# Performance work log

Measured on AMD Instinct MI355X. Metric: run time of the kernel, lower is better.

## Reference

```python
import jax, jax.numpy as jnp
import numpy as np


def _pe_2d(H, W, C, dtype):
    # PositionalEncodingPermute2D: returns (C, H, W)
    ch_half = (C + 1) // 2
    inv = 1.0 / (10000.0 ** (jnp.arange(0, ch_half, 2, dtype=jnp.float32) / ch_half))
    tH = jnp.arange(H, dtype=jnp.float32)
    tW = jnp.arange(W, dtype=jnp.float32)
    sinH = tH[:, None] * inv[None, :]              # (H, ch_half//2)
    sinW = tW[:, None] * inv[None, :]              # (W, ch_half//2)
    embH = jnp.concatenate([jnp.sin(sinH), jnp.cos(sinH)], axis=-1)  # (H, ch_half)
    embW = jnp.concatenate([jnp.sin(sinW), jnp.cos(sinW)], axis=-1)  # (W, ch_half)
    E = jnp.concatenate([
        jnp.broadcast_to(embW[None, :, :], (H, W, ch_half)),
        jnp.broadcast_to(embH[:, None, :], (H, W, ch_half)),
    ], axis=-1)[..., :C]                            # (H, W, C)
    return jnp.transpose(E, (2, 0, 1)).astype(dtype)  # (C, H, W)


def setup_inputs() -> dict:
    key = jax.random.key(0)
    k0, k1, k2, k3 = jax.random.split(key, 4)
    B, C, H, W = 4, 256, 64, 64
    s = 1.0 / np.sqrt(C)  # kaiming-ish scale
    return {
        "x": jax.random.normal(k0, (B, C, H, W), dtype=jnp.float32),
        "wq": jax.random.normal(k1, (C, C), dtype=jnp.float32) * s,
        "wk": jax.random.normal(k2, (C, C), dtype=jnp.float32) * s,
        "wv": jax.random.normal(k3, (C, C), dtype=jnp.float32) * s,
    }


def reference(x, wq, wk, wv):
    B, C, H, W = x.shape
    scale = C ** (-0.5)
    x = x + _pe_2d(H, W, C, x.dtype)[None]          # (B, C, H, W)
    X = x.reshape(B, C, H * W).transpose(0, 2, 1)   # (B, N, C)
    Q = jnp.einsum('bnc,dc->bnd', X, wq)
    K = jnp.einsum('bnc,dc->bnd', X, wk)
    V = jnp.einsum('bnc,dc->bnd', X, wv)
    A = jax.nn.softmax(jnp.einsum('bnd,bmd->bnm', Q, K) * scale, axis=-1)
    Y = jnp.einsum('bnm,bmd->bnd', A, V)            # (B, N, C)
    return Y.transpose(0, 2, 1).reshape(B, C, H, W)
```

## Files before the change

### kernel.cpp

```cpp
#include <hip/hip_runtime.h>
#include <hip/hip_bf16.h>

#define BB 4
#define CC 256
#define NN 4096
#define NSPLIT 4
#define KSPLIT (NN / NSPLIT)
#define NPAIR (KSPLIT / 64)

typedef __attribute__((ext_vector_type(8))) short short8;
typedef __attribute__((ext_vector_type(4))) float floatx4;
typedef __attribute__((ext_vector_type(4))) unsigned short ushortx4;

__device__ __forceinline__ float bf2f(unsigned short u) {
  union { unsigned int i; float f; } cv; cv.i = ((unsigned int)u) << 16; return cv.f;
}
__device__ __forceinline__ unsigned short f2bf(float f) {
  union { __hip_bfloat16 h; unsigned short u; } cv; cv.h = __float2bfloat16(f); return cv.u;
}

#define MFMA(a, b, c) __builtin_amdgcn_mfma_f32_16x16x32_bf16((a), (b), (c), 0, 0, 0)

__device__ __forceinline__ void dma16(const unsigned short* g, unsigned short* l) {
  __builtin_amdgcn_global_load_lds(
      (const __attribute__((address_space(1))) unsigned int*)g,
      (__attribute__((address_space(3))) unsigned int*)l, 16, 0, 0);
}
#define S_BARRIER __builtin_amdgcn_s_barrier()
#define MEMFENCE __asm__ volatile("" ::: "memory")

__global__ __launch_bounds__(256) void wcvt(const float* __restrict__ w0,
                                            const float* __restrict__ w1,
                                            const float* __restrict__ w2,
                                            unsigned short* __restrict__ o0,
                                            unsigned short* __restrict__ o1,
                                            unsigned short* __restrict__ o2) {
  const float* w = (blockIdx.y == 0) ? w0 : (blockIdx.y == 1) ? w1 : w2;
  unsigned short* o = (blockIdx.y == 0) ? o0 : (blockIdx.y == 1) ? o1 : o2;
  int i = (blockIdx.x * 256 + threadIdx.x) * 4;
  floatx4 v = *(const floatx4*)&w[i];
  ushortx4 p;
#pragma unroll
  for (int r = 0; r < 4; r++) p[r] = f2bf(v[r]);
  *(ushortx4*)&o[i] = p;
}

__global__ __launch_bounds__(256) void prep_x(const float* __restrict__ x,
                                              unsigned short* __restrict__ Xbf) {
  __shared__ float tile[32][33];
  int b = blockIdx.z;
  int n0 = blockIdx.x * 32, c0 = blockIdx.y * 32;
  int tx = threadIdx.x, ty = threadIdx.y;
#pragma unroll
  for (int i = 0; i < 4; i++) {
    int c = c0 + ty + i * 8;
    int n = n0 + tx;
    float v = x[((long)(b * CC + c)) * NN + n];
    int hh = n >> 6, ww = n & 63;
    int j = c & 63;
    float freq = exp2f(-0.2076205059304601f * (float)j);
    float arg = (float)((c < 128) ? ww : hh) * freq;
    v += (c & 64) ? cosf(arg) : sinf(arg);
    tile[ty + i * 8][tx] = v;
  }
  __syncthreads();
#pragma unroll
  for (int i = 0; i < 4; i++) {
    int n = n0 + ty + i * 8;
    int c = c0 + tx;
    Xbf[((long)(b * NN + n)) * CC + c] = f2bf(tile[tx][ty + i * 8]);
  }
}

__global__ __launch_bounds__(256, 2) void gemm_fused(const unsigned short* __restrict__ Xbf,
                                                     const unsigned short* __restrict__ Wqk,
                                                     const unsigned short* __restrict__ Wv,
                                                     unsigned short* __restrict__ QK,
                                                     unsigned short* __restrict__ Vt) {
  __shared__ alignas(16) unsigned short Af[2][8 * 512];
  __shared__ alignas(16) unsigned short Bf[2][8 * 512];
  const unsigned short *Ab, *Bb;
  unsigned short* Ob;
  long row0, col0;
  int ldo;
  int F = blockIdx.x;
  if (F < 512) {
    int b = F >> 7, r = F & 127;
    row0 = (long)(r >> 2) * 128;
    col0 = (long)(r & 3) * 128;
    Ab = Xbf + (long)b * NN * CC;
    Bb = Wqk;
    Ob = QK + (long)b * NN * 512;
    ldo = 512;
  } else {
    int F2 = F - 512;
    int b = F2 >> 6, r = F2 & 63;
    row0 = (long)(r >> 5) * 128;
    col0 = (long)(r & 31) * 128;
    Ab = Wv;
    Bb = Xbf + (long)b * NN * CC;
    Ob = Vt + (long)b * CC * NN;
    ldo = NN;
  }
  int t = threadIdx.x, wave = t >> 6, lane = t & 63, quad = lane >> 4, l15 = lane & 15;
  int wr = wave >> 1, wc = wave & 1;

  auto stage = [&](int k0, int buf) {
#pragma unroll
    for (int i = 0; i < 2; i++) {
      int fg = wave * 2 + i;
      dma16(&Ab[(row0 + fg * 16 + l15) * 256 + k0 + quad * 8], &Af[buf][fg * 512]);
      dma16(&Bb[(col0 + fg * 16 + l15) * 256 + k0 + quad * 8], &Bf[buf][fg * 512]);
    }
  };

  floatx4 acc[4][4] = {};
  stage(0, 0);
  MEMFENCE;
#pragma unroll
  for (int ki = 0; ki < 8; ki++) {
    int buf = ki & 1;
    S_BARRIER;
    MEMFENCE;
    if (ki + 1 < 8) {
      stage((ki + 1) * 32, buf ^ 1);
      MEMFENCE;
      __builtin_amdgcn_s_waitcnt(0xF74);
    } else {
      __builtin_amdgcn_s_waitcnt(0xF70);
    }
    S_BARRIER;
    MEMFENCE;
    short8 af[4], bf[4];
#pragma unroll
    for (int i = 0; i < 4; i++) {
      af[i] = *(const short8*)&Af[buf][(wr * 4 + i) * 512 + lane * 8];
      bf[i] = *(const short8*)&Bf[buf][(wc * 4 + i) * 512 + lane * 8];
    }
#pragma unroll
    for (int i = 0; i < 4; i++)
#pragma unroll
      for (int j = 0; j < 4; j++) acc[i][j] = MFMA(af[i], bf[j], acc[i][j]);
  }

#pragma unroll
  for (int i = 0; i < 4; i++)
#pragma unroll
    for (int j = 0; j < 4; j++) {
      long col = col0 + (wc * 4 + j) * 16 + l15;
#pragma unroll
      for (int r = 0; r < 4; r++) {
        long row = row0 + (wr * 4 + i) * 16 + quad * 4 + r;
        Ob[row * (long)ldo + col] = f2bf(acc[i][j][r]);
      }
    }
}

__global__ __launch_bounds__(512, 1) void attn(const unsigned short* __restrict__ QKg,
                                               const unsigned short* __restrict__ Vtg,
                                               unsigned short* __restrict__ Opart,
                                               float* __restrict__ Lp) {
  __shared__ alignas(16) unsigned short Kl[4 * 8192];
  __shared__ alignas(16) unsigned short Vl[4 * 8192];
  __shared__ alignas(16) unsigned short Plf[8][2][512];
  int F = blockIdx.x;
  int c = F & 15, sp = c & 3, b = c >> 2;
  long q0 = (long)(F >> 4) * 256;
  int t = threadIdx.x, wave = t >> 6, lane = t & 63, quad = lane >> 4, l15 = lane & 15;
  const unsigned short* Qb = QKg + (long)b * NN * 512;
  const unsigned short* Kb = Qb + 256;
  const unsigned short* Vb = Vtg + (long)b * CC * NN;

  short8 qf[2][8];
#pragma unroll
  for (int qb = 0; qb < 2; qb++) {
    long qrow = q0 + wave * 32 + qb * 16 + l15;
#pragma unroll
    for (int ks = 0; ks < 8; ks++)
      qf[qb][ks] = *(const short8*)&Qb[qrow * 512 + ks * 32 + quad * 8];
  }

  floatx4 acc[2][17] = {};
  short8 ones;
#pragma unroll
  for (int j = 0; j < 8; j++) ones[j] = (short)0x3F80;

  const float sc = 0.0625f * 1.4426950408889634f;
  const int kbeg = sp * KSPLIT;

  auto stage_pair = [&](int p, int buf) {
#pragma unroll
    for (int tt = 0; tt < 2; tt++) {
      int m0 = kbeg + (p * 2 + tt) * 32;
      int slot = buf * 2 + tt;
#pragma unroll
      for (int st = 0; st < 2; st++) {
        int fg = st * 8 + wave;
        dma16(&Kb[(long)(m0 + st * 16 + l15) * 512 + wave * 32 + quad * 8],
              &Kl[slot * 8192 + fg * 512]);
        dma16(&Vb[(long)(fg * 16 + l15) * NN + m0 + quad * 8],
              &Vl[slot * 8192 + fg * 512]);
      }
    }
  };

  __builtin_amdgcn_s_waitcnt(0xF70);
  stage_pair(0, 0);
  MEMFENCE;

  for (int p = 0; p < NPAIR; p++) {
    int buf = p & 1;
    S_BARRIER;
    MEMFENCE;
    if (p + 1 < NPAIR) {
      stage_pair(p + 1, buf ^ 1);
      MEMFENCE;
      __builtin_amdgcn_s_waitcnt(0xF78);
    } else {
      __builtin_amdgcn_s_waitcnt(0xF70);
    }
    S_BARRIER;
    MEMFENCE;

#pragma unroll
    for (int tt = 0; tt < 2; tt++) {
      int kb = (buf * 2 + tt) * 8192;
      floatx4 s[2][2];
      {
        floatx4 z = {0.f, 0.f, 0.f, 0.f};
        s[0][0] = z; s[0][1] = z; s[1][0] = z; s[1][1] = z;
      }
#pragma unroll
      for (int fgk = 0; fgk < 16; fgk++) {
        short8 kf = *(const short8*)&Kl[kb + fgk * 512 + lane * 8];
        int mt = fgk >> 3, ks = fgk & 7;
        s[0][mt] = MFMA(qf[0][ks], kf, s[0][mt]);
        s[1][mt] = MFMA(qf[1][ks], kf, s[1][mt]);
      }

#pragma unroll
      for (int qb = 0; qb < 2; qb++) {
#pragma unroll
        for (int r = 0; r < 4; r++) {
          unsigned short pb0 = f2bf(__builtin_amdgcn_exp2f(s[qb][0][r] * sc));
          unsigned short pb1 = f2bf(__builtin_amdgcn_exp2f(s[qb][1][r] * sc));
          int m = quad * 4 + r;
          Plf[wave][qb][((l15 >> 3) * 16 + m) * 8 + (l15 & 7)] = pb0;
          Plf[wave][qb][((2 + (l15 >> 3)) * 16 + m) * 8 + (l15 & 7)] = pb1;
        }
      }
      MEMFENCE;
      short8 pf0 = *(const short8*)&Plf[wave][0][lane * 8];
      short8 pf1 = *(const short8*)&Plf[wave][1][lane * 8];
      acc[0][16] = MFMA(pf0, ones, acc[0][16]);
      acc[1][16] = MFMA(pf1, ones, acc[1][16]);
#pragma unroll
      for (int db = 0; db < 16; db++) {
        short8 vf = *(const short8*)&Vl[kb + db * 512 + lane * 8];
        acc[0][db] = MFMA(pf0, vf, acc[0][db]);
        acc[1][db] = MFMA(pf1, vf, acc[1][db]);
      }
      MEMFENCE;
    }
  }

  unsigned short* Ob = Opart + (long)(b * NSPLIT + sp) * CC * NN;
#pragma unroll
  for (int qb = 0; qb < 2; qb++) {
    long nidx = q0 + wave * 32 + qb * 16 + quad * 4;
#pragma unroll
    for (int db = 0; db < 16; db++) {
      long d = db * 16 + l15;
      ushortx4 pk;
#pragma unroll
      for (int r = 0; r < 4; r++) pk[r] = f2bf(acc[qb][db][r]);
      *(ushortx4*)&Ob[d * NN + nidx] = pk;
    }
    if (l15 == 0) {
#pragma unroll
      for (int r = 0; r < 4; r++)
        Lp[(long)(b * NSPLIT + sp) * NN + nidx + r] = acc[qb][16][r];
    }
  }
}

__global__ __launch_bounds__(256) void combine(const unsigned short* __restrict__ Op,
                                               const float* __restrict__ Lp,
                                               float* __restrict__ Out) {
  __shared__ float Wl[64];
  int b = blockIdx.z;
  int d0 = blockIdx.y * 64, n0 = blockIdx.x * 64;
  int t = threadIdx.x;
  if (t < 64) {
    int n = n0 + t;
    float L = 0.f;
#pragma unroll
    for (int s = 0; s < NSPLIT; s++) L += Lp[(long)(b * NSPLIT + s) * NN + n];
    Wl[t] = 1.0f / L;
  }
  __syncthreads();
  int tn = t & 15, td = t >> 4;
  int nb = n0 + tn * 4;
  float w[4];
#pragma unroll
  for (int r = 0; r < 4; r++) w[r] = Wl[tn * 4 + r];
#pragma unroll
  for (int dd = 0; dd < 4; dd++) {
    int d = d0 + td * 4 + dd;
    floatx4 o = {0.f, 0.f, 0.f, 0.f};
#pragma unroll
    for (int s = 0; s < NSPLIT; s++) {
      ushortx4 pv = *(const ushortx4*)&Op[((long)(b * NSPLIT + s) * CC + d) * NN + nb];
#pragma unroll
      for (int r = 0; r < 4; r++) o[r] += bf2f(pv[r]);
    }
#pragma unroll
    for (int r = 0; r < 4; r++) o[r] *= w[r];
    *(floatx4*)&Out[((long)b * CC + d) * NN + nb] = o;
  }
}

extern "C" void kernel_launch(void* const* d_in, const int* in_sizes, int n_in,
                              void* d_out, int out_size, void* d_ws, size_t ws_size,
                              hipStream_t stream) {
  const float* x = (const float*)d_in[0];
  const float* wq = (const float*)d_in[1];
  const float* wk = (const float*)d_in[2];
  const float* wv = (const float*)d_in[3];
  float* out = (float*)d_out;

  char* ws = (char*)d_ws;
  unsigned short* QKbuf = (unsigned short*)(ws);
  unsigned short* Vt = (unsigned short*)(ws + (16l << 20));
  unsigned short* Xbf = (unsigned short*)(ws + (24l << 20));
  unsigned short* Opart = (unsigned short*)(ws + (24l << 20));
  float* Lp = (float*)(ws + (56l << 20));
  unsigned short* Wqk = (unsigned short*)(ws + (57l << 20));
  unsigned short* Wv = (unsigned short*)(ws + (57l << 20) + (1 << 19));

  wcvt<<<dim3(CC * CC / 1024, 3), 256, 0, stream>>>(wq, wk, wv, Wqk, Wqk + CC * CC, Wv);
  prep_x<<<dim3(NN / 32, CC / 32, BB), dim3(32, 8), 0, stream>>>(x, Xbf);
  gemm_fused<<<dim3(768), 256, 0, stream>>>(Xbf, Wqk, Wv, QKbuf, Vt);
  attn<<<dim3(256), 512, 0, stream>>>(QKbuf, Vt, Opart, Lp);
  combine<<<dim3(NN / 64, CC / 64, BB), 256, 0, stream>>>(Opart, Lp, out);
}
```

Measured before the change: 194.1 us.

## Fuse weight conversion into prep_x and split-K combine into attn via counters

Weight fp32-to-bf16 conversion moves into the first 192 blocks of prep_x, which also zeroes a set of arrival counters. This removes the separate wcvt launch. The combine kernel is folded into the end of attn: each block increments a per-query-tile counter, spins until all four split blocks have arrived, then reduces its own 64-channel slice of the partial outputs and normalizes. This saves two kernel launches and their tails. The cost is an inter-block spin wait that relies on all 256 one-per-CU blocks being co-resident.

```diff
diff --git a/kernel.cpp b/kernel.cpp
--- a/kernel.cpp
+++ b/kernel.cpp
@@ -29,24 +29,38 @@
 #define S_BARRIER __builtin_amdgcn_s_barrier()
 #define MEMFENCE __asm__ volatile("" ::: "memory")
 
-__global__ __launch_bounds__(256) void wcvt(const float* __restrict__ w0,
-                                            const float* __restrict__ w1,
-                                            const float* __restrict__ w2,
-                                            unsigned short* __restrict__ o0,
-                                            unsigned short* __restrict__ o1,
-                                            unsigned short* __restrict__ o2) {
-  const float* w = (blockIdx.y == 0) ? w0 : (blockIdx.y == 1) ? w1 : w2;
-  unsigned short* o = (blockIdx.y == 0) ? o0 : (blockIdx.y == 1) ? o1 : o2;
-  int i = (blockIdx.x * 256 + threadIdx.x) * 4;
-  floatx4 v = *(const floatx4*)&w[i];
-  ushortx4 p;
-#pragma unroll
-  for (int r = 0; r < 4; r++) p[r] = f2bf(v[r]);
-  *(ushortx4*)&o[i] = p;
-}
-
 __global__ __launch_bounds__(256) void prep_x(const float* __restrict__ x,
-                                              unsigned short* __restrict__ Xbf) {
+                                              const float* __restrict__ wq,
+                                              const float* __restrict__ wk,
+                                              const float* __restrict__ wv,
+                                              unsigned short* __restrict__ Xbf,
+                                              unsigned short* __restrict__ Wqk,
+                                              unsigned short* __restrict__ Wv,
+                                              int* __restrict__ cnt) {
+  int tid = threadIdx.y * 32 + threadIdx.x;
+  int gid = blockIdx.x + gridDim.x * (blockIdx.y + gridDim.y * blockIdx.z);
+  if (gid < 192) {
+    int e = gid * 1024 + tid * 4;
+    floatx4 v;
+    unsigned short* dst;
+    if (e < 65536) {
+      v = *(const floatx4*)&wq[e];
+      dst = &Wqk[e];
+    } else if (e < 131072) {
+      v = *(const floatx4*)&wk[e - 65536];
+      dst = &Wqk[e];
+    } else {
+      v = *(const floatx4*)&wv[e - 131072];
+      dst = &Wv[e - 131072];
+    }
+    ushortx4 p;
+#pragma unroll
+    for (int r = 0; r < 4; r++) p[r] = f2bf(v[r]);
+    *(ushortx4*)dst = p;
+  } else if (gid == 192 && tid < 64) {
+    cnt[tid] = 0;
+  }
+
   __shared__ float tile[32][33];
   int b = blockIdx.z;
   int n0 = blockIdx.x * 32, c0 = blockIdx.y * 32;
@@ -159,13 +173,16 @@
 __global__ __launch_bounds__(512, 1) void attn(const unsigned short* __restrict__ QKg,
                                                const unsigned short* __restrict__ Vtg,
                                                unsigned short* __restrict__ Opart,
-                                               float* __restrict__ Lp) {
+                                               float* __restrict__ Lp,
+                                               float* __restrict__ Out,
+                                               int* __restrict__ cnt) {
   __shared__ alignas(16) unsigned short Kl[4 * 8192];
   __shared__ alignas(16) unsigned short Vl[4 * 8192];
   __shared__ alignas(16) unsigned short Plf[8][2][512];
   int F = blockIdx.x;
   int c = F & 15, sp = c & 3, b = c >> 2;
-  long q0 = (long)(F >> 4) * 256;
+  int qt = F >> 4;
+  long q0 = (long)qt * 256;
   int t = threadIdx.x, wave = t >> 6, lane = t & 63, quad = lane >> 4, l15 = lane & 15;
   const unsigned short* Qb = QKg + (long)b * NN * 512;
   const unsigned short* Kb = Qb + 256;
@@ -282,41 +299,44 @@
         Lp[(long)(b * NSPLIT + sp) * NN + nidx + r] = acc[qb][16][r];
     }
   }
-}
-
-__global__ __launch_bounds__(256) void combine(const unsigned short* __restrict__ Op,
-                                               const float* __restrict__ Lp,
-                                               float* __restrict__ Out) {
-  __shared__ float Wl[64];
-  int b = blockIdx.z;
-  int d0 = blockIdx.y * 64, n0 = blockIdx.x * 64;
-  int t = threadIdx.x;
-  if (t < 64) {
-    int n = n0 + t;
+
+  int grp = b * 16 + qt;
+  __syncthreads();
+  if (t == 0) {
+    __threadfence();
+    atomicAdd(&cnt[grp], 1);
+    while (__hip_atomic_load(&cnt[grp], __ATOMIC_ACQUIRE,
+                             __HIP_MEMORY_SCOPE_AGENT) < NSPLIT)
+      __builtin_amdgcn_s_sleep(8);
+  }
+  __syncthreads();
+  __threadfence();
+
+  float* invL = (float*)Plf;
+  if (t < 256) {
     float L = 0.f;
 #pragma unroll
-    for (int s = 0; s < NSPLIT; s++) L += Lp[(long)(b * NSPLIT + s) * NN + n];
-    Wl[t] = 1.0f / L;
+    for (int s = 0; s < NSPLIT; s++) L += Lp[(long)(b * NSPLIT + s) * NN + q0 + t];
+    invL[t] = 1.0f / L;
   }
   __syncthreads();
-  int tn = t & 15, td = t >> 4;
-  int nb = n0 + tn * 4;
-  float w[4];
-#pragma unroll
-  for (int r = 0; r < 4; r++) w[r] = Wl[tn * 4 + r];
-#pragma unroll
-  for (int dd = 0; dd < 4; dd++) {
-    int d = d0 + td * 4 + dd;
+
+  const unsigned short* Opb = Opart + (long)b * NSPLIT * CC * NN;
+  int dbase = sp * 64 + (t >> 6) * 8;
+  int n4 = (t & 63) * 4;
+#pragma unroll
+  for (int dd = 0; dd < 8; dd++) {
+    int d = dbase + dd;
     floatx4 o = {0.f, 0.f, 0.f, 0.f};
 #pragma unroll
     for (int s = 0; s < NSPLIT; s++) {
-      ushortx4 pv = *(const ushortx4*)&Op[((long)(b * NSPLIT + s) * CC + d) * NN + nb];
+      ushortx4 pv = *(const ushortx4*)&Opb[((long)s * CC + d) * NN + q0 + n4];
 #pragma unroll
       for (int r = 0; r < 4; r++) o[r] += bf2f(pv[r]);
     }
 #pragma unroll
-    for (int r = 0; r < 4; r++) o[r] *= w[r];
-    *(floatx4*)&Out[((long)b * CC + d) * NN + nb] = o;
+    for (int r = 0; r < 4; r++) o[r] *= invL[n4 + r];
+    *(floatx4*)&Out[((long)b * CC + d) * NN + q0 + n4] = o;
   }
 }
 
@@ -337,10 +357,10 @@
   float* Lp = (float*)(ws + (56l << 20));
   unsigned short* Wqk = (unsigned short*)(ws + (57l << 20));
   unsigned short* Wv = (unsigned short*)(ws + (57l << 20) + (1 << 19));
-
-  wcvt<<<dim3(CC * CC / 1024, 3), 256, 0, stream>>>(wq, wk, wv, Wqk, Wqk + CC * CC, Wv);
-  prep_x<<<dim3(NN / 32, CC / 32, BB), dim3(32, 8), 0, stream>>>(x, Xbf);
+  int* cnt = (int*)(ws + (57l << 20) + (1 << 19) + (1 << 18));
+
+  prep_x<<<dim3(NN / 32, CC / 32, BB), dim3(32, 8), 0, stream>>>(x, wq, wk, wv, Xbf,
+                                                                 Wqk, Wv, cnt);
   gemm_fused<<<dim3(768), 256, 0, stream>>>(Xbf, Wqk, Wv, QKbuf, Vt);
-  attn<<<dim3(256), 512, 0, stream>>>(QKbuf, Vt, Opart, Lp);
-  combine<<<dim3(NN / 64, CC / 64, BB), 256, 0, stream>>>(Opart, Lp, out);
-}
+  attn<<<dim3(256), 512, 0, stream>>>(QKbuf, Vt, Opart, Lp, out, cnt);
+}
```

After: 233.6 us. 20.4% more time.

## Halve attention waves with four query tiles per wave; fold weight cast into prep

Applied to the files above, without the earlier changes.

The attention kernel now runs 4 waves per block instead of 8, and each wave handles 64 query rows (four 16-row tiles). Each K and V fragment read from LDS is therefore reused across four MFMAs, which cuts LDS read traffic per FLOP. The cost is many more accumulator registers (68 floatx4 plus Q fragments) and fewer waves to hide latency, and the K/V staging and waitcnt are adjusted to match. Separately, the weight bf16 conversion is merged into the prep_x kernel to save one launch.

```diff
diff --git a/kernel.cpp b/kernel.cpp
--- a/kernel.cpp
+++ b/kernel.cpp
@@ -29,24 +29,35 @@
 #define S_BARRIER __builtin_amdgcn_s_barrier()
 #define MEMFENCE __asm__ volatile("" ::: "memory")
 
-__global__ __launch_bounds__(256) void wcvt(const float* __restrict__ w0,
-                                            const float* __restrict__ w1,
-                                            const float* __restrict__ w2,
-                                            unsigned short* __restrict__ o0,
-                                            unsigned short* __restrict__ o1,
-                                            unsigned short* __restrict__ o2) {
-  const float* w = (blockIdx.y == 0) ? w0 : (blockIdx.y == 1) ? w1 : w2;
-  unsigned short* o = (blockIdx.y == 0) ? o0 : (blockIdx.y == 1) ? o1 : o2;
-  int i = (blockIdx.x * 256 + threadIdx.x) * 4;
-  floatx4 v = *(const floatx4*)&w[i];
-  ushortx4 p;
-#pragma unroll
-  for (int r = 0; r < 4; r++) p[r] = f2bf(v[r]);
-  *(ushortx4*)&o[i] = p;
-}
-
 __global__ __launch_bounds__(256) void prep_x(const float* __restrict__ x,
-                                              unsigned short* __restrict__ Xbf) {
+                                              const float* __restrict__ wq,
+                                              const float* __restrict__ wk,
+                                              const float* __restrict__ wv,
+                                              unsigned short* __restrict__ Xbf,
+                                              unsigned short* __restrict__ Wqk,
+                                              unsigned short* __restrict__ Wv) {
+  int tid = threadIdx.y * 32 + threadIdx.x;
+  int gid = blockIdx.x + gridDim.x * (blockIdx.y + gridDim.y * blockIdx.z);
+  if (gid < 192) {
+    int e = gid * 1024 + tid * 4;
+    floatx4 v;
+    unsigned short* dst;
+    if (e < 65536) {
+      v = *(const floatx4*)&wq[e];
+      dst = &Wqk[e];
+    } else if (e < 131072) {
+      v = *(const floatx4*)&wk[e - 65536];
+      dst = &Wqk[e];
+    } else {
+      v = *(const floatx4*)&wv[e - 131072];
+      dst = &Wv[e - 131072];
+    }
+    ushortx4 p;
+#pragma unroll
+    for (int r = 0; r < 4; r++) p[r] = f2bf(v[r]);
+    *(ushortx4*)dst = p;
+  }
+
   __shared__ float tile[32][33];
   int b = blockIdx.z;
   int n0 = blockIdx.x * 32, c0 = blockIdx.y * 32;
@@ -156,13 +167,13 @@
     }
 }
 
-__global__ __launch_bounds__(512, 1) void attn(const unsigned short* __restrict__ QKg,
+__global__ __launch_bounds__(256, 1) void attn(const unsigned short* __restrict__ QKg,
                                                const unsigned short* __restrict__ Vtg,
                                                unsigned short* __restrict__ Opart,
                                                float* __restrict__ Lp) {
   __shared__ alignas(16) unsigned short Kl[4 * 8192];
   __shared__ alignas(16) unsigned short Vl[4 * 8192];
-  __shared__ alignas(16) unsigned short Plf[8][2][512];
+  __shared__ alignas(16) unsigned short Plf[4][4][512];
   int F = blockIdx.x;
   int c = F & 15, sp = c & 3, b = c >> 2;
   long q0 = (long)(F >> 4) * 256;
@@ -171,16 +182,16 @@
   const unsigned short* Kb = Qb + 256;
   const unsigned short* Vb = Vtg + (long)b * CC * NN;
 
-  short8 qf[2][8];
-#pragma unroll
-  for (int qb = 0; qb < 2; qb++) {
-    long qrow = q0 + wave * 32 + qb * 16 + l15;
+  short8 qf[4][8];
+#pragma unroll
+  for (int qb = 0; qb < 4; qb++) {
+    long qrow = q0 + wave * 64 + qb * 16 + l15;
 #pragma unroll
     for (int ks = 0; ks < 8; ks++)
       qf[qb][ks] = *(const short8*)&Qb[qrow * 512 + ks * 32 + quad * 8];
   }
 
-  floatx4 acc[2][17] = {};
+  floatx4 acc[4][17] = {};
   short8 ones;
 #pragma unroll
   for (int j = 0; j < 8; j++) ones[j] = (short)0x3F80;
@@ -194,9 +205,9 @@
       int m0 = kbeg + (p * 2 + tt) * 32;
       int slot = buf * 2 + tt;
 #pragma unroll
-      for (int st = 0; st < 2; st++) {
-        int fg = st * 8 + wave;
-        dma16(&Kb[(long)(m0 + st * 16 + l15) * 512 + wave * 32 + quad * 8],
+      for (int st = 0; st < 4; st++) {
+        int fg = st * 4 + wave;
+        dma16(&Kb[(long)(m0 + (fg >> 3) * 16 + l15) * 512 + (fg & 7) * 32 + quad * 8],
               &Kl[slot * 8192 + fg * 512]);
         dma16(&Vb[(long)(fg * 16 + l15) * NN + m0 + quad * 8],
               &Vl[slot * 8192 + fg * 512]);
@@ -215,7 +226,7 @@
     if (p + 1 < NPAIR) {
       stage_pair(p + 1, buf ^ 1);
       MEMFENCE;
-      __builtin_amdgcn_s_waitcnt(0xF78);
+      __builtin_amdgcn_s_waitcnt(0x4F70);
     } else {
       __builtin_amdgcn_s_waitcnt(0xF70);
     }
@@ -225,21 +236,23 @@
 #pragma unroll
     for (int tt = 0; tt < 2; tt++) {
       int kb = (buf * 2 + tt) * 8192;
-      floatx4 s[2][2];
-      {
+      floatx4 s[4][2];
+#pragma unroll
+      for (int qb = 0; qb < 4; qb++) {
         floatx4 z = {0.f, 0.f, 0.f, 0.f};
-        s[0][0] = z; s[0][1] = z; s[1][0] = z; s[1][1] = z;
+        s[qb][0] = z;
+        s[qb][1] = z;
       }
 #pragma unroll
       for (int fgk = 0; fgk < 16; fgk++) {
         short8 kf = *(const short8*)&Kl[kb + fgk * 512 + lane * 8];
         int mt = fgk >> 3, ks = fgk & 7;
-        s[0][mt] = MFMA(qf[0][ks], kf, s[0][mt]);
-        s[1][mt] = MFMA(qf[1][ks], kf, s[1][mt]);
-      }
-
-#pragma unroll
-      for (int qb = 0; qb < 2; qb++) {
+#pragma unroll
+        for (int qb = 0; qb < 4; qb++) s[qb][mt] = MFMA(qf[qb][ks], kf, s[qb][mt]);
+      }
+
+#pragma unroll
+      for (int qb = 0; qb < 4; qb++) {
 #pragma unroll
         for (int r = 0; r < 4; r++) {
           unsigned short pb0 = f2bf(__builtin_amdgcn_exp2f(s[qb][0][r] * sc));
@@ -250,15 +263,17 @@
         }
       }
       MEMFENCE;
-      short8 pf0 = *(const short8*)&Plf[wave][0][lane * 8];
-      short8 pf1 = *(const short8*)&Plf[wave][1][lane * 8];
-      acc[0][16] = MFMA(pf0, ones, acc[0][16]);
-      acc[1][16] = MFMA(pf1, ones, acc[1][16]);
+      short8 pf[4];
+#pragma unroll
+      for (int qb = 0; qb < 4; qb++) {
+        pf[qb] = *(const short8*)&Plf[wave][qb][lane * 8];
+        acc[qb][16] = MFMA(pf[qb], ones, acc[qb][16]);
+      }
 #pragma unroll
       for (int db = 0; db < 16; db++) {
         short8 vf = *(const short8*)&Vl[kb + db * 512 + lane * 8];
-        acc[0][db] = MFMA(pf0, vf, acc[0][db]);
-        acc[1][db] = MFMA(pf1, vf, acc[1][db]);
+#pragma unroll
+        for (int qb = 0; qb < 4; qb++) acc[qb][db] = MFMA(pf[qb], vf, acc[qb][db]);
       }
       MEMFENCE;
     }
@@ -266,8 +281,8 @@
 
   unsigned short* Ob = Opart + (long)(b * NSPLIT + sp) * CC * NN;
 #pragma unroll
-  for (int qb = 0; qb < 2; qb++) {
-    long nidx = q0 + wave * 32 + qb * 16 + quad * 4;
+  for (int qb = 0; qb < 4; qb++) {
+    long nidx = q0 + wave * 64 + qb * 16 + quad * 4;
 #pragma unroll
     for (int db = 0; db < 16; db++) {
       long d = db * 16 + l15;
@@ -338,9 +353,9 @@
   unsigned short* Wqk = (unsigned short*)(ws + (57l << 20));
   unsigned short* Wv = (unsigned short*)(ws + (57l << 20) + (1 << 19));
 
-  wcvt<<<dim3(CC * CC / 1024, 3), 256, 0, stream>>>(wq, wk, wv, Wqk, Wqk + CC * CC, Wv);
-  prep_x<<<dim3(NN / 32, CC / 32, BB), dim3(32, 8), 0, stream>>>(x, Xbf);
+  prep_x<<<dim3(NN / 32, CC / 32, BB), dim3(32, 8), 0, stream>>>(x, wq, wk, wv, Xbf,
+                                                                 Wqk, Wv);
   gemm_fused<<<dim3(768), 256, 0, stream>>>(Xbf, Wqk, Wv, QKbuf, Vt);
-  attn<<<dim3(256), 512, 0, stream>>>(QKbuf, Vt, Opart, Lp);
+  attn<<<dim3(256), 256, 0, stream>>>(QKbuf, Vt, Opart, Lp);
   combine<<<dim3(NN / 64, CC / 64, BB), 256, 0, stream>>>(Opart, Lp, out);
 }
```

New measurement: 489.9 us. 2.52x slower.

## Fold weight conversion into prep_x and software-pipeline QK/PV in attention

Applied to the files above, without the earlier changes.

Removes the separate weight-conversion kernel by having the first 192 blocks of prep_x also convert wq/wk/wv to bf16, saving one launch. In the attention inner loop, the two sub-tiles are reordered so the QK MFMAs of the second tile are issued before the PV MFMAs of the first. This lets exp/softmax writes and MFMA chains overlap. The reorder keeps the S registers of one tile live across the other tile's work, which may raise register pressure. It also relies on the single per-wave P buffer being read before it is overwritten, with only compiler fences and no barrier between them.

```diff
diff --git a/kernel.cpp b/kernel.cpp
--- a/kernel.cpp
+++ b/kernel.cpp
@@ -29,24 +29,35 @@
 #define S_BARRIER __builtin_amdgcn_s_barrier()
 #define MEMFENCE __asm__ volatile("" ::: "memory")
 
-__global__ __launch_bounds__(256) void wcvt(const float* __restrict__ w0,
-                                            const float* __restrict__ w1,
-                                            const float* __restrict__ w2,
-                                            unsigned short* __restrict__ o0,
-                                            unsigned short* __restrict__ o1,
-                                            unsigned short* __restrict__ o2) {
-  const float* w = (blockIdx.y == 0) ? w0 : (blockIdx.y == 1) ? w1 : w2;
-  unsigned short* o = (blockIdx.y == 0) ? o0 : (blockIdx.y == 1) ? o1 : o2;
-  int i = (blockIdx.x * 256 + threadIdx.x) * 4;
-  floatx4 v = *(const floatx4*)&w[i];
-  ushortx4 p;
-#pragma unroll
-  for (int r = 0; r < 4; r++) p[r] = f2bf(v[r]);
-  *(ushortx4*)&o[i] = p;
-}
-
 __global__ __launch_bounds__(256) void prep_x(const float* __restrict__ x,
-                                              unsigned short* __restrict__ Xbf) {
+                                              const float* __restrict__ wq,
+                                              const float* __restrict__ wk,
+                                              const float* __restrict__ wv,
+                                              unsigned short* __restrict__ Xbf,
+                                              unsigned short* __restrict__ Wqk,
+                                              unsigned short* __restrict__ Wv) {
+  int tid = threadIdx.y * 32 + threadIdx.x;
+  int gid = blockIdx.x + gridDim.x * (blockIdx.y + gridDim.y * blockIdx.z);
+  if (gid < 192) {
+    int e = gid * 1024 + tid * 4;
+    floatx4 v;
+    unsigned short* dst;
+    if (e < 65536) {
+      v = *(const floatx4*)&wq[e];
+      dst = &Wqk[e];
+    } else if (e < 131072) {
+      v = *(const floatx4*)&wk[e - 65536];
+      dst = &Wqk[e];
+    } else {
+      v = *(const floatx4*)&wv[e - 131072];
+      dst = &Wv[e - 131072];
+    }
+    ushortx4 p;
+#pragma unroll
+    for (int r = 0; r < 4; r++) p[r] = f2bf(v[r]);
+    *(ushortx4*)dst = p;
+  }
+
   __shared__ float tile[32][33];
   int b = blockIdx.z;
   int n0 = blockIdx.x * 32, c0 = blockIdx.y * 32;
@@ -204,6 +215,47 @@
     }
   };
 
+  auto qk = [&](int kb, floatx4 s[2][2]) {
+#pragma unroll
+    for (int qb = 0; qb < 2; qb++) {
+      floatx4 z = {0.f, 0.f, 0.f, 0.f};
+      s[qb][0] = z;
+      s[qb][1] = z;
+    }
+#pragma unroll
+    for (int fgk = 0; fgk < 16; fgk++) {
+      short8 kf = *(const short8*)&Kl[kb + fgk * 512 + lane * 8];
+      int mt = fgk >> 3, ks = fgk & 7;
+      s[0][mt] = MFMA(qf[0][ks], kf, s[0][mt]);
+      s[1][mt] = MFMA(qf[1][ks], kf, s[1][mt]);
+    }
+  };
+  auto expwr = [&](floatx4 s[2][2]) {
+#pragma unroll
+    for (int qb = 0; qb < 2; qb++) {
+#pragma unroll
+      for (int r = 0; r < 4; r++) {
+        unsigned short pb0 = f2bf(__builtin_amdgcn_exp2f(s[qb][0][r] * sc));
+        unsigned short pb1 = f2bf(__builtin_amdgcn_exp2f(s[qb][1][r] * sc));
+        int m = quad * 4 + r;
+        Plf[wave][qb][((l15 >> 3) * 16 + m) * 8 + (l15 & 7)] = pb0;
+        Plf[wave][qb][((2 + (l15 >> 3)) * 16 + m) * 8 + (l15 & 7)] = pb1;
+      }
+    }
+  };
+  auto pv = [&](int kb) {
+    short8 pf0 = *(const short8*)&Plf[wave][0][lane * 8];
+    short8 pf1 = *(const short8*)&Plf[wave][1][lane * 8];
+    acc[0][16] = MFMA(pf0, ones, acc[0][16]);
+    acc[1][16] = MFMA(pf1, ones, acc[1][16]);
+#pragma unroll
+    for (int db = 0; db < 16; db++) {
+      short8 vf = *(const short8*)&Vl[kb + db * 512 + lane * 8];
+      acc[0][db] = MFMA(pf0, vf, acc[0][db]);
+      acc[1][db] = MFMA(pf1, vf, acc[1][db]);
+    }
+  };
+
   __builtin_amdgcn_s_waitcnt(0xF70);
   stage_pair(0, 0);
   MEMFENCE;
@@ -222,46 +274,16 @@
     S_BARRIER;
     MEMFENCE;
 
-#pragma unroll
-    for (int tt = 0; tt < 2; tt++) {
-      int kb = (buf * 2 + tt) * 8192;
-      floatx4 s[2][2];
-      {
-        floatx4 z = {0.f, 0.f, 0.f, 0.f};
-        s[0][0] = z; s[0][1] = z; s[1][0] = z; s[1][1] = z;
-      }
-#pragma unroll
-      for (int fgk = 0; fgk < 16; fgk++) {
-        short8 kf = *(const short8*)&Kl[kb + fgk * 512 + lane * 8];
-        int mt = fgk >> 3, ks = fgk & 7;
-        s[0][mt] = MFMA(qf[0][ks], kf, s[0][mt]);
-        s[1][mt] = MFMA(qf[1][ks], kf, s[1][mt]);
-      }
-
-#pragma unroll
-      for (int qb = 0; qb < 2; qb++) {
-#pragma unroll
-        for (int r = 0; r < 4; r++) {
-          unsigned short pb0 = f2bf(__builtin_amdgcn_exp2f(s[qb][0][r] * sc));
-          unsigned short pb1 = f2bf(__builtin_amdgcn_exp2f(s[qb][1][r] * sc));
-          int m = quad * 4 + r;
-          Plf[wave][qb][((l15 >> 3) * 16 + m) * 8 + (l15 & 7)] = pb0;
-          Plf[wave][qb][((2 + (l15 >> 3)) * 16 + m) * 8 + (l15 & 7)] = pb1;
-        }
-      }
-      MEMFENCE;
-      short8 pf0 = *(const short8*)&Plf[wave][0][lane * 8];
-      short8 pf1 = *(const short8*)&Plf[wave][1][lane * 8];
-      acc[0][16] = MFMA(pf0, ones, acc[0][16]);
-      acc[1][16] = MFMA(pf1, ones, acc[1][16]);
-#pragma unroll
-      for (int db = 0; db < 16; db++) {
-        short8 vf = *(const short8*)&Vl[kb + db * 512 + lane * 8];
-        acc[0][db] = MFMA(pf0, vf, acc[0][db]);
-        acc[1][db] = MFMA(pf1, vf, acc[1][db]);
-      }
-      MEMFENCE;
-    }
+    int kb0 = (buf * 2) * 8192, kb1 = kb0 + 8192;
+    floatx4 s[2][2];
+    qk(kb0, s);
+    expwr(s);
+    qk(kb1, s);
+    MEMFENCE;
+    pv(kb0);
+    expwr(s);
+    MEMFENCE;
+    pv(kb1);
   }
 
   unsigned short* Ob = Opart + (long)(b * NSPLIT + sp) * CC * NN;
@@ -338,8 +360,8 @@
   unsigned short* Wqk = (unsigned short*)(ws + (57l << 20));
   unsigned short* Wv = (unsigned short*)(ws + (57l << 20) + (1 << 19));
 
-  wcvt<<<dim3(CC * CC / 1024, 3), 256, 0, stream>>>(wq, wk, wv, Wqk, Wqk + CC * CC, Wv);
-  prep_x<<<dim3(NN / 32, CC / 32, BB), dim3(32, 8), 0, stream>>>(x, Xbf);
+  prep_x<<<dim3(NN / 32, CC / 32, BB), dim3(32, 8), 0, stream>>>(x, wq, wk, wv, Xbf,
+                                                                 Wqk, Wv);
   gemm_fused<<<dim3(768), 256, 0, stream>>>(Xbf, Wqk, Wv, QKbuf, Vt);
   attn<<<dim3(256), 512, 0, stream>>>(QKbuf, Vt, Opart, Lp);
   combine<<<dim3(NN / 64, CC / 64, BB), 256, 0, stream>>>(Opart, Lp, out);
```

Measured after the change: 197.4 us. About the same (+1.7%).
